# Optimization experiments

Measured on AMD Instinct MI355X. Metric: run time of the kernel, lower is better.

The kernel has to match this reference:

```python
import jax, jax.numpy as jnp
import numpy as np

N_HEADS = 16


def _rope_table(seq_len, head_dim):
    # Matches RotaryPositionalEmbedding: emb = cat(sin(pos*inv_freq), cos(pos*inv_freq))
    inv_freq = 1.0 / (10000.0 ** (jnp.arange(0, head_dim, 2, dtype=jnp.float32) / head_dim))
    sinusoid = jnp.arange(seq_len, dtype=jnp.float32)[:, None] * inv_freq[None, :]  # [S, hd/2]
    return jnp.sin(sinusoid), jnp.cos(sinusoid)


def _apply_rope(q, k, seq_len, head_dim):
    # Faithful to the torch code, which slices emb[:, :hd/2] (== sin) and calls it 'cos',
    # and emb[:, hd/2:] (== cos) and calls it 'sin'. We keep that exact math.
    sin_tab, cos_tab = _rope_table(seq_len, head_dim)
    c = sin_tab[None, None]  # named 'cos' in torch code, actually sin values
    s = cos_tab[None, None]  # named 'sin' in torch code, actually cos values
    half = head_dim // 2
    def rot(x):
        x1, x2 = x[..., :half], x[..., half:]
        return jnp.concatenate([x1 * c - x2 * s, x2 * c + x1 * s], axis=-1)
    return rot(q), rot(k)


def setup_inputs() -> dict:
    key = jax.random.key(0)
    ks = jax.random.split(key, 9)
    B, S, D = 4, 2048, 1024
    sc = 1.0 / np.sqrt(D)
    return {
        'hidden_states': jax.random.normal(ks[0], (B, S, D), jnp.float32),
        'Wq': jax.random.normal(ks[1], (D, D), jnp.float32) * sc,
        'bq': jax.random.normal(ks[2], (D,), jnp.float32) * 0.01,
        'Wk': jax.random.normal(ks[3], (D, D), jnp.float32) * sc,
        'bk': jax.random.normal(ks[4], (D,), jnp.float32) * 0.01,
        'Wv': jax.random.normal(ks[5], (D, D), jnp.float32) * sc,
        'bv': jax.random.normal(ks[6], (D,), jnp.float32) * 0.01,
        'Wo': jax.random.normal(ks[7], (D, D), jnp.float32) * sc,
        'bo': jax.random.normal(ks[8], (D,), jnp.float32) * 0.01,
    }


def reference(hidden_states, Wq, bq, Wk, bk, Wv, bv, Wo, bo):
    B, S, D = hidden_states.shape
    H = N_HEADS
    hd = D // H

    def proj(W, b):
        y = jnp.einsum('bsd,ed->bse', hidden_states, W) + b  # nn.Linear: x @ W.T + b
        return y.reshape(B, S, H, hd).transpose(0, 2, 1, 3)   # [B,H,S,hd]

    q = proj(Wq, bq)
    k = proj(Wk, bk)
    v = proj(Wv, bv)
    q, k = _apply_rope(q, k, S, hd)

    scale = 1.0 / np.sqrt(hd)
    scores = jnp.einsum('bhqd,bhkd->bhqk', q, k) * scale  # [B,H,S,S]
    attn = jax.nn.softmax(scores, axis=-1)
    ctx = jnp.einsum('bhqk,bhkd->bhqd', attn, v)          # [B,H,S,hd]
    ctx = ctx.transpose(0, 2, 1, 3).reshape(B, S, D)
    return jnp.einsum('bsd,ed->bse', ctx, Wo) + bo
```

## Files before the change

kernel.cpp:

```cpp
#include <hip/hip_runtime.h>
#include <math.h>

#define SEQ 2048
#define DMODEL 1024
#define NH 16
#define HD 64
#define BH 64
#define MROWS 8192
#define QKV_U16 8388608
#define LOG2E 1.4426950408889634f

typedef __attribute__((ext_vector_type(8))) _Float16 half8;
typedef __attribute__((ext_vector_type(4))) _Float16 half4;
typedef __attribute__((ext_vector_type(2))) __fp16 fp16v2;
typedef __attribute__((ext_vector_type(8))) short short8;
typedef __attribute__((ext_vector_type(4))) float floatx4;
typedef unsigned short ush;

union FH { _Float16 h; ush u; };
union PK { fp16v2 v; unsigned u; };
union PH { unsigned u[2]; half4 h; };

__device__ inline ush f2h(float x) { FH c; c.h = (_Float16)x; return c.u; }

__global__ __launch_bounds__(256)
void cvt_kb(const float* __restrict__ src, ush* __restrict__ dst, int M) {
  __shared__ float T[64][33];
  const int t = threadIdx.x;
  const int k0 = blockIdx.x * 32, m0 = blockIdx.y * 64;
  {
    int row = t >> 2, c = (t & 3) * 8;
    const float* sp = src + (size_t)(m0 + row) * DMODEL + k0 + c;
    float4 x0 = *(const float4*)sp;
    float4 x1 = *(const float4*)(sp + 4);
    float xs[8] = {x0.x, x0.y, x0.z, x0.w, x1.x, x1.y, x1.z, x1.w};
#pragma unroll
    for (int j = 0; j < 8; ++j) T[row][c + j] = xs[j];
  }
  __syncthreads();
  const int ml = t & 63, kbl = t >> 6;
  short8 h8;
#pragma unroll
  for (int j = 0; j < 8; ++j) h8[j] = (short)f2h(T[ml][kbl * 8 + j]);
  *(short8*)(dst + ((size_t)(k0 / 8 + kbl) * M + m0 + ml) * 8) = h8;
}

__global__ __launch_bounds__(256)
void cvt_w4(const float* __restrict__ W0, const float* __restrict__ W1,
            const float* __restrict__ W2, const float* __restrict__ W3,
            ush* __restrict__ dst) {
  __shared__ float T[64][33];
  const int z = blockIdx.z;
  const float* src = (z == 0) ? W0 : (z == 1) ? W1 : (z == 2) ? W2 : W3;
  ush* dz = dst + (size_t)z * DMODEL * DMODEL;
  const int t = threadIdx.x;
  const int k0 = blockIdx.x * 32, m0 = blockIdx.y * 64;
  {
    int row = t >> 2, c = (t & 3) * 8;
    const float* sp = src + (size_t)(m0 + row) * DMODEL + k0 + c;
    float4 x0 = *(const float4*)sp;
    float4 x1 = *(const float4*)(sp + 4);
    float xs[8] = {x0.x, x0.y, x0.z, x0.w, x1.x, x1.y, x1.z, x1.w};
#pragma unroll
    for (int j = 0; j < 8; ++j) T[row][c + j] = xs[j];
  }
  __syncthreads();
  const int ml = t & 63, kbl = t >> 6;
  short8 h8;
#pragma unroll
  for (int j = 0; j < 8; ++j) h8[j] = (short)f2h(T[ml][kbl * 8 + j]);
  *(short8*)(dz + ((size_t)(k0 / 8 + kbl) * DMODEL + m0 + ml) * 8) = h8;
}

__global__ __launch_bounds__(256)
void sincos_kernel(float2* __restrict__ tab) {
  const int idx = blockIdx.x * 256 + threadIdx.x;
  const int s = idx >> 5, i = idx & 31;
  const float f = (float)pow(10000.0, -(double)i / 32.0);
  const float ang = (float)s * f;
  tab[idx] = make_float2(sinf(ang), cosf(ang));
}

template<int TGT>
__global__ __launch_bounds__(256, 2)
void gemm_f16(const ush* __restrict__ A, const ush* __restrict__ W,
              const float* __restrict__ bias, void* __restrict__ outp,
              const float2* __restrict__ sctab, float scale) {
  const int tid  = threadIdx.x;
  const int wave = tid >> 6;
  const int lane = tid & 63;
  const int fr = lane & 15;
  const int fg = lane >> 4;
  const int wm = wave & 1;
  const int wn = wave >> 1;
  const int m_base = blockIdx.y * 128 + wm * 64;
  const int n_base = blockIdx.x * 128 + wn * 64;

  floatx4 acc[4][4];
#pragma unroll
  for (int i = 0; i < 4; ++i)
#pragma unroll
    for (int j = 0; j < 4; ++j) acc[i][j] = (floatx4){0.f, 0.f, 0.f, 0.f};

  const ush* Abase = A + (size_t)(m_base + fr) * 8;
  const ush* Wbase = W + (size_t)(n_base + fr) * 8;

  auto gload = [&](half8 (&ah)[2][4], half8 (&wh)[2][4], int kt) {
#pragma unroll
    for (int ks = 0; ks < 2; ++ks) {
      const int kb = (kt >> 3) + ks * 4 + fg;
      const ush* ap = Abase + (size_t)kb * (MROWS * 8);
      const ush* wp = Wbase + (size_t)kb * (DMODEL * 8);
#pragma unroll
      for (int t = 0; t < 4; ++t) {
        ah[ks][t] = *(const half8*)(ap + t * 128);
        wh[ks][t] = *(const half8*)(wp + t * 128);
      }
    }
  };
  auto kstep = [&](const half8 (&ah)[2][4], const half8 (&wh)[2][4]) {
#pragma unroll
    for (int ks = 0; ks < 2; ++ks)
#pragma unroll
      for (int tm = 0; tm < 4; ++tm)
#pragma unroll
        for (int tn = 0; tn < 4; ++tn)
          acc[tm][tn] = __builtin_amdgcn_mfma_f32_16x16x32_f16(ah[ks][tm], wh[ks][tn], acc[tm][tn], 0, 0, 0);
  };

  half8 ahA[2][4], whA[2][4], ahB[2][4], whB[2][4];
  gload(ahA, whA, 0);
  for (int kt = 0; kt < DMODEL; kt += 128) {
    gload(ahB, whB, kt + 64);
    kstep(ahA, whA);
    if (kt + 128 < DMODEL) gload(ahA, whA, kt + 128);
    kstep(ahB, whB);
  }

  float bias_s[4];
#pragma unroll
  for (int tn = 0; tn < 4; ++tn) bias_s[tn] = bias[n_base + tn * 16 + fr];

  if (TGT == 3) {
#pragma unroll
    for (int tm = 0; tm < 4; ++tm)
#pragma unroll
      for (int tn = 0; tn < 4; ++tn)
#pragma unroll
        for (int r = 0; r < 4; ++r) {
          const int m = m_base + tm * 16 + fg * 4 + r;
          const int n = n_base + tn * 16 + fr;
          ((float*)outp)[(size_t)m * DMODEL + n] = acc[tm][tn][r] + bias_s[tn];
        }
    return;
  }

  const int h = (n_base >> 6) & 15;
  ush* out = (ush*)outp;

  if (TGT == 2) {
#pragma unroll
    for (int tm = 0; tm < 4; ++tm)
#pragma unroll
      for (int tn = 0; tn < 4; ++tn)
#pragma unroll
        for (int r = 0; r < 4; ++r) {
          const int m = m_base + tm * 16 + fg * 4 + r;
          const int s = m & (SEQ - 1);
          const size_t bh = (size_t)((m >> 11) * NH + h);
          const int d = tn * 16 + fr;
          const int k6 = s & 63, ktl = s >> 6;
          const int s2 = k6 >> 5;
          const int jj = ((k6 >> 4) & 1) * 4 + (k6 & 3);
          const int fgv = (k6 >> 2) & 3;
          const int dt = d >> 4, frv = d & 15;
          size_t pos = ((((bh * 32 + ktl) * 4 + dt) * 2 + s2) * 64 + fgv * 16 + frv) * 8 + jj;
          out[pos] = f2h(acc[tm][tn][r] + bias_s[tn]);
        }
    return;
  }

#pragma unroll
  for (int tn2 = 0; tn2 < 2; ++tn2) {
    const int i = tn2 * 16 + fr;
#pragma unroll
    for (int tm = 0; tm < 4; ++tm)
#pragma unroll
      for (int r = 0; r < 4; ++r) {
        const int m = m_base + tm * 16 + fg * 4 + r;
        const int s = m & (SEQ - 1);
        const size_t bh = (size_t)((m >> 11) * NH + h);
        const float x1 = acc[tm][tn2][r] + bias_s[tn2];
        const float x2 = acc[tm][tn2 + 2][r] + bias_s[tn2 + 2];
        const float2 sc = sctab[(s << 5) + i];
        const float sv = sc.x, cv = sc.y;
        const float o1 = (x1 * sv - x2 * cv) * scale;
        const float o2 = (x2 * sv + x1 * cv) * scale;
        const int d1 = i, d2 = i + 32;
#pragma unroll
        for (int e = 0; e < 2; ++e) {
          const int d = e ? d2 : d1;
          const float ov = e ? o2 : o1;
          const int ks = d >> 5, fgq = (d >> 3) & 3, j = d & 7;
          size_t pos;
          if (TGT == 0) {
            const int qt = s >> 5, mm = (s >> 4) & 1, fr2 = s & 15;
            pos = ((((bh * 64 + qt) * 2 + mm) * 2 + ks) * 64 + fgq * 16 + fr2) * 8 + j;
          } else {
            const int ktl = s >> 6, jt = (s >> 4) & 3, fr2 = s & 15;
            pos = ((((bh * 32 + ktl) * 4 + jt) * 2 + ks) * 64 + fgq * 16 + fr2) * 8 + j;
          }
          out[pos] = f2h(ov);
        }
      }
  }
}

__global__ __launch_bounds__(256, 2)
void flash_mfma(const ush* __restrict__ qsw, const ush* __restrict__ ksw,
                const ush* __restrict__ vsw, ush* __restrict__ ctxf) {
  __shared__ __align__(16) ush Tep[4][64][72];
  __shared__ float Lden[4][64];
  const int tid = threadIdx.x;
  const int wave = tid >> 6;
  const int lane = tid & 63;
  const int fr = lane & 15;
  const int fg = lane >> 4;

  const int lin = blockIdx.x + 8 * blockIdx.y;
  const int xcd = lin & 7;
  const int t2  = lin >> 3;
  const int qblk = t2 & 7;
  const int bh   = xcd + 8 * (t2 >> 3);

  const int q0 = qblk * 256 + wave * 64;
  const ush* qp = qsw + ((size_t)bh * 64 + (q0 >> 5)) * 2048;
  const ush* kp = ksw + (size_t)bh * 131072;
  const ush* vp = vsw + (size_t)bh * 131072;

  half8 qf[4][2];
#pragma unroll
  for (int qn = 0; qn < 4; ++qn)
#pragma unroll
    for (int ks = 0; ks < 2; ++ks)
      qf[qn][ks] = *(const half8*)(qp + (qn * 2 + ks) * 512 + lane * 8);

  floatx4 oacc[4][4];
#pragma unroll
  for (int qn = 0; qn < 4; ++qn)
#pragma unroll
    for (int i = 0; i < 4; ++i) oacc[qn][i] = (floatx4){0.f, 0.f, 0.f, 0.f};
  float lsum[4] = {0.f, 0.f, 0.f, 0.f};

  const fp16v2 one2 = {(__fp16)1.0f, (__fp16)1.0f};

  for (int kt = 0; kt < 32; ++kt) {
    const ush* ktp = kp + kt * 4096;
    const ush* vtp = vp + kt * 4096;

    half8 kf[8], vf[8];
#pragma unroll
    for (int i = 0; i < 8; ++i) kf[i] = *(const half8*)(ktp + i * 512 + lane * 8);
#pragma unroll
    for (int i = 0; i < 8; ++i) vf[i] = *(const half8*)(vtp + i * 512 + lane * 8);

#pragma unroll
    for (int qn = 0; qn < 4; ++qn) {
      floatx4 s4[4];
#pragma unroll
      for (int jt = 0; jt < 4; ++jt) s4[jt] = (floatx4){0.f, 0.f, 0.f, 0.f};
#pragma unroll
      for (int ks = 0; ks < 2; ++ks)
#pragma unroll
        for (int jt = 0; jt < 4; ++jt)
          s4[jt] = __builtin_amdgcn_mfma_f32_16x16x32_f16(kf[jt * 2 + ks], qf[qn][ks], s4[jt], 0, 0, 0);

      half4 P[4];
#pragma unroll
      for (int jt = 0; jt < 4; ++jt) {
        float p0 = __builtin_amdgcn_exp2f(s4[jt][0]);
        float p1 = __builtin_amdgcn_exp2f(s4[jt][1]);
        float p2 = __builtin_amdgcn_exp2f(s4[jt][2]);
        float p3 = __builtin_amdgcn_exp2f(s4[jt][3]);
        PK a, b;
        a.v = __builtin_amdgcn_cvt_pkrtz(p0, p1);
        b.v = __builtin_amdgcn_cvt_pkrtz(p2, p3);
        lsum[qn] = __builtin_amdgcn_fdot2(a.v, one2, lsum[qn], false);
        lsum[qn] = __builtin_amdgcn_fdot2(b.v, one2, lsum[qn], false);
        PH ph; ph.u[0] = a.u; ph.u[1] = b.u;
        P[jt] = ph.h;
      }

#pragma unroll
      for (int sub = 0; sub < 4; ++sub) {
        const int s2 = sub >> 1, hk = sub & 1;
#pragma unroll
        for (int dt = 0; dt < 4; ++dt) {
          half8 v8 = vf[dt * 2 + s2];
          half4 vs = hk ? __builtin_shufflevector(v8, v8, 4, 5, 6, 7)
                        : __builtin_shufflevector(v8, v8, 0, 1, 2, 3);
          oacc[qn][dt] = __builtin_amdgcn_mfma_f32_16x16x16f16(P[sub], vs, oacc[qn][dt], 0, 0, 0);
        }
      }
    }
  }

#pragma unroll
  for (int qn = 0; qn < 4; ++qn) {
    lsum[qn] += __shfl_xor(lsum[qn], 16);
    lsum[qn] += __shfl_xor(lsum[qn], 32);
    Lden[wave][qn * 16 + fr] = lsum[qn];
  }

  const int b = bh >> 4, h = bh & 15;
#pragma unroll
  for (int qn = 0; qn < 4; ++qn)
#pragma unroll
    for (int r = 0; r < 4; ++r) {
      const float inv = 1.0f / Lden[wave][qn * 16 + fg * 4 + r];
#pragma unroll
      for (int dt = 0; dt < 4; ++dt)
        Tep[wave][qn * 16 + fg * 4 + r][dt * 16 + fr] = f2h(oacc[qn][dt][r] * inv);
    }
  const size_t mrow0 = (size_t)b * SEQ + q0;
  const int kb = lane >> 3;
#pragma unroll
  for (int i = 0; i < 8; ++i) {
    const int q = (lane & 7) + i * 8;
    short8 v = *(const short8*)&Tep[wave][q][kb * 8];
    *(short8*)(ctxf + ((size_t)(h * 8 + kb) * MROWS + mrow0 + q) * 8) = v;
  }
}

extern "C" void kernel_launch(void* const* d_in, const int* in_sizes, int n_in,
                              void* d_out, int out_size, void* d_ws, size_t ws_size,
                              hipStream_t stream) {
  const float* hs = (const float*)d_in[0];
  const float* Wq = (const float*)d_in[1];
  const float* bq = (const float*)d_in[2];
  const float* Wk = (const float*)d_in[3];
  const float* bk = (const float*)d_in[4];
  const float* Wv = (const float*)d_in[5];
  const float* bv = (const float*)d_in[6];
  const float* Wo = (const float*)d_in[7];
  const float* bo = (const float*)d_in[8];

  ush* qsw  = (ush*)d_ws;
  ush* ksw  = qsw + QKV_U16;
  ush* vsw  = ksw + QKV_U16;
  ush* hsf  = vsw + QKV_U16;
  ush* ctxf = hsf + QKV_U16;
  ush* Wf4  = ctxf + QKV_U16;
  float2* sctab = (float2*)(Wf4 + 4 * DMODEL * DMODEL);

  const size_t WS = (size_t)DMODEL * DMODEL;

  sincos_kernel<<<256, 256, 0, stream>>>(sctab);
  cvt_w4<<<dim3(32, 16, 4), 256, 0, stream>>>(Wq, Wk, Wv, Wo, Wf4);
  cvt_kb<<<dim3(32, 128), 256, 0, stream>>>(hs, hsf, MROWS);

  dim3 gridG(DMODEL / 128, MROWS / 128);
  gemm_f16<0><<<gridG, 256, 0, stream>>>(hsf, Wf4 + 0 * WS, bq, qsw, sctab, 0.125f * LOG2E);
  gemm_f16<1><<<gridG, 256, 0, stream>>>(hsf, Wf4 + 1 * WS, bk, ksw, sctab, 1.0f);
  gemm_f16<2><<<gridG, 256, 0, stream>>>(hsf, Wf4 + 2 * WS, bv, vsw, sctab, 1.0f);

  flash_mfma<<<dim3(8, BH), 256, 0, stream>>>(qsw, ksw, vsw, ctxf);

  gemm_f16<3><<<gridG, 256, 0, stream>>>(ctxf, Wf4 + 3 * WS, bo, d_out, sctab, 1.0f);
}
```

Measured before the change: 316.0 us.

## Stage GEMM tiles through LDS with direct global-to-LDS loads, double-buffered

The f16 GEMM no longer has each wave load its own A/W fragments straight from global memory into registers. The block now cooperatively copies 128x64 tiles of A and W into double-buffered shared memory with global_load_lds, and waves read their fragments from LDS. This cuts redundant global traffic, since the 2x2 waves previously each reloaded shared rows, and frees registers. The cost is 64KB of LDS per block, which may limit occupancy to two blocks per CU, plus a block barrier each k-step.

```diff
diff --git a/kernel.cpp b/kernel.cpp
--- a/kernel.cpp
+++ b/kernel.cpp
@@ -22,6 +22,11 @@
 union PH { unsigned u[2]; half4 h; };
 
 __device__ inline ush f2h(float x) { FH c; c.h = (_Float16)x; return c.u; }
+
+__device__ inline void glds16(const ush* g, ush* l) {
+  __builtin_amdgcn_global_load_lds((const __attribute__((address_space(1))) void*)g,
+                                   (__attribute__((address_space(3))) void*)l, 16, 0, 0);
+}
 
 __global__ __launch_bounds__(256)
 void cvt_kb(const float* __restrict__ src, ush* __restrict__ dst, int M) {
@@ -86,6 +91,8 @@
 void gemm_f16(const ush* __restrict__ A, const ush* __restrict__ W,
               const float* __restrict__ bias, void* __restrict__ outp,
               const float2* __restrict__ sctab, float scale) {
+  __shared__ ush SA[2][8192];
+  __shared__ ush SW[2][8192];
   const int tid  = threadIdx.x;
   const int wave = tid >> 6;
   const int lane = tid & 63;
@@ -93,8 +100,10 @@
   const int fg = lane >> 4;
   const int wm = wave & 1;
   const int wn = wave >> 1;
-  const int m_base = blockIdx.y * 128 + wm * 64;
-  const int n_base = blockIdx.x * 128 + wn * 64;
+  const int m0 = blockIdx.y * 128;
+  const int n0 = blockIdx.x * 128;
+  const int m_base = m0 + wm * 64;
+  const int n_base = n0 + wn * 64;
 
   floatx4 acc[4][4];
 #pragma unroll
@@ -102,39 +111,43 @@
 #pragma unroll
     for (int j = 0; j < 4; ++j) acc[i][j] = (floatx4){0.f, 0.f, 0.f, 0.f};
 
-  const ush* Abase = A + (size_t)(m_base + fr) * 8;
-  const ush* Wbase = W + (size_t)(n_base + fr) * 8;
-
-  auto gload = [&](half8 (&ah)[2][4], half8 (&wh)[2][4], int kt) {
-#pragma unroll
-    for (int ks = 0; ks < 2; ++ks) {
-      const int kb = (kt >> 3) + ks * 4 + fg;
-      const ush* ap = Abase + (size_t)kb * (MROWS * 8);
-      const ush* wp = Wbase + (size_t)kb * (DMODEL * 8);
-#pragma unroll
-      for (int t = 0; t < 4; ++t) {
-        ah[ks][t] = *(const half8*)(ap + t * 128);
-        wh[ks][t] = *(const half8*)(wp + t * 128);
-      }
+  auto stage = [&](int b, int kb0) {
+#pragma unroll
+    for (int p = 0; p < 4; ++p) {
+      const int eb = p * 256 + wave * 64;
+      const int kb = eb >> 7, r0 = eb & 127;
+      const ush* ga = A + (size_t)(kb0 + kb) * (MROWS * 8) + (size_t)(m0 + r0 + lane) * 8;
+      glds16(ga, &SA[b][(size_t)eb * 8]);
+      const ush* gw = W + (size_t)(kb0 + kb) * (DMODEL * 8) + (size_t)(n0 + r0 + lane) * 8;
+      glds16(gw, &SW[b][(size_t)eb * 8]);
     }
   };
-  auto kstep = [&](const half8 (&ah)[2][4], const half8 (&wh)[2][4]) {
-#pragma unroll
-    for (int ks = 0; ks < 2; ++ks)
+
+  auto compute = [&](int b) {
+#pragma unroll
+    for (int ks = 0; ks < 2; ++ks) {
+      const int kbl = ks * 4 + fg;
+      half8 ah[4], wh[4];
 #pragma unroll
       for (int tm = 0; tm < 4; ++tm)
+        ah[tm] = *(const half8*)&SA[b][(size_t)(kbl * 128 + wm * 64 + tm * 16 + fr) * 8];
+#pragma unroll
+      for (int tn = 0; tn < 4; ++tn)
+        wh[tn] = *(const half8*)&SW[b][(size_t)(kbl * 128 + wn * 64 + tn * 16 + fr) * 8];
+#pragma unroll
+      for (int tm = 0; tm < 4; ++tm)
 #pragma unroll
         for (int tn = 0; tn < 4; ++tn)
-          acc[tm][tn] = __builtin_amdgcn_mfma_f32_16x16x32_f16(ah[ks][tm], wh[ks][tn], acc[tm][tn], 0, 0, 0);
+          acc[tm][tn] = __builtin_amdgcn_mfma_f32_16x16x32_f16(ah[tm], wh[tn], acc[tm][tn], 0, 0, 0);
+    }
   };
 
-  half8 ahA[2][4], whA[2][4], ahB[2][4], whB[2][4];
-  gload(ahA, whA, 0);
-  for (int kt = 0; kt < DMODEL; kt += 128) {
-    gload(ahB, whB, kt + 64);
-    kstep(ahA, whA);
-    if (kt + 128 < DMODEL) gload(ahA, whA, kt + 128);
-    kstep(ahB, whB);
+  stage(0, 0);
+  __syncthreads();
+  for (int t = 0; t < 16; ++t) {
+    if (t + 1 < 16) stage((t + 1) & 1, (t + 1) * 8);
+    compute(t & 1);
+    __syncthreads();
   }
 
   float bias_s[4];
```

New measurement: 298.9 us. -5.4%, faster.
